# Kernel optimization log

Measured on AMD Instinct MI355X. Metric: run time of the kernel, lower is better.

Reference implementation:

```python
import jax, jax.numpy as jnp
import numpy as np

# Geometry of the single LocallyConnected2d layer being decomposed
FACTOR = 2      # number of sublayers the out_channels are split into
KH = KW = 3     # kernel size
DH = DW = 1     # stride
OH = OW = 32    # output spatial size
B, C_IN, C_OUT = 128, 32, 64
H = W = OH + KH - 1  # 34 (valid unfold with stride 1)


def setup_inputs() -> dict:
    key = jax.random.key(0)
    kx, kw_, kb = jax.random.split(key, 3)
    x = jax.random.normal(kx, (B, C_IN, H, W), dtype=jnp.float32)
    # per-location weights: (out_ch, in_ch, oh, ow, kh*kw) -- no weight sharing
    weight = jax.random.normal(kw_, (C_OUT, C_IN, OH, OW, KH * KW), dtype=jnp.float32) * 0.05
    bias = jax.random.normal(kb, (C_OUT, OH, OW), dtype=jnp.float32)
    return {"x": x, "weight": weight, "bias": bias}


def _unfold(x):
    # x: (B, C, H, W) -> patches: (B, C, OH, OW, KH*KW)
    # equivalent to torch x.unfold(2,kh,dh).unfold(3,kw,dw).reshape(..., kh*kw)
    cols = [x[:, :, i:i + DH * OH:DH, j:j + DW * OW:DW]
            for i in range(KH) for j in range(KW)]
    return jnp.stack(cols, axis=-1)


def reference(x, weight, bias):
    patches = _unfold(x)  # (B, C, OH, OW, K2)
    new_ch = weight.shape[0] // FACTOR
    outs = []
    for g in range(FACTOR):  # decomposed sublayers, concatenated on channel dim
        w_g = weight[g * new_ch:(g + 1) * new_ch]
        b_g = bias[g * new_ch:(g + 1) * new_ch]
        # out[b,o,i,j] = sum_{c,k} patches[b,c,i,j,k] * w[o,c,i,j,k] + b[o,i,j]
        o_g = jnp.einsum('bcijk,ocijk->boij', patches, w_g) + b_g[None]
        outs.append(o_g)
    return jnp.concatenate(outs, axis=1)  # (B, C_OUT, OH, OW)
```

## Files before the change

kernel.cpp:

```cpp
#include <hip/hip_runtime.h>
#include <cstdint>
#include <cstddef>

#define B_    128
#define C_    32
#define O_    64
#define H_    34
#define NPOS  1024
#define K9    9
#define BC    (B_ * C_)
#define BO    (B_ * O_)

typedef __bf16 v8bf __attribute__((ext_vector_type(8)));
typedef float  v4f  __attribute__((ext_vector_type(4)));
typedef float  f4a  __attribute__((ext_vector_type(4)));

__device__ __forceinline__ unsigned short f2bf(float f) {
    union { float f; unsigned int u; } v; v.f = f;
    unsigned int u = v.u;
    return (unsigned short)((u + 0x7FFFu + ((u >> 16) & 1u)) >> 16);
}

__global__ __launch_bounds__(256) void repack_x(const float* __restrict__ x,
                                                unsigned short* __restrict__ x2) {
    const int bq = blockIdx.x / 17;
    const int hp = blockIdx.x % 17;
    const int b0 = bq * 2;
    const int h0 = hp * 2;
    __shared__ unsigned short tile[2][H_][66];
    const int t = threadIdx.x;

    for (int e = t; e < 2176; e += 256) {
        const int bb  = e / 1088;
        const int rem = e % 1088;
        const int c   = rem / 34;
        const int wp  = rem % 34;
        const float2 v = *(const float2*)(x +
            ((size_t)((b0 + bb) * C_ + c) * H_ + h0) * H_ + wp * 2);
        const int hh = (wp >= 17) ? 1 : 0;
        const int w  = wp * 2 - hh * 34;
        const int idx = bb * 32 + c;
        tile[hh][w][idx]     = f2bf(v.x);
        tile[hh][w + 1][idx] = f2bf(v.y);
    }
    __syncthreads();

    for (int e = t; e < 2176; e += 256) {
        const int hh  = e / 1088;
        const int rem = e % 1088;
        const int w   = rem >> 5;
        const int i2  = rem & 31;
        ushort2 pk;
        pk.x = tile[hh][w][i2 * 2];
        pk.y = tile[hh][w][i2 * 2 + 1];
        *(ushort2*)(x2 + (size_t)((h0 + hh) * H_ + w) * BC + bq * 64 + i2 * 2) = pk;
    }
}

__global__ __launch_bounds__(256, 2) void lc_fused2(const unsigned short* __restrict__ x2,
                                                    const float* __restrict__ weight,
                                                    const float* __restrict__ bias,
                                                    float* __restrict__ out) {
    __shared__ __align__(16) unsigned short Wl[72 * 512];

    const int bid = blockIdx.x;
    const int lb  = (bid & 7) * 64 + (bid >> 3);
    const int i   = lb >> 4;
    const int jq  = (lb >> 2) & 3;
    const int oq  = lb & 3;
    const int j0  = jq * 8;
    const int o0  = oq * 16;
    const int posbase = i * 32 + j0;
    const int t = threadIdx.x;

    const float* wbase = weight + ((size_t)(o0 * C_) * NPOS + posbase) * K9;
#pragma unroll
    for (int r = 0; r < 9; ++r) {
        const int idx = r * 256 + t;
        const int plq = idx / 18;
        const int d4  = idx % 18;
        f4a v0 = *(const f4a*)(wbase + (size_t)(plq * 4 + 0) * (NPOS * K9) + d4 * 4);
        f4a v1 = *(const f4a*)(wbase + (size_t)(plq * 4 + 1) * (NPOS * K9) + d4 * 4);
        f4a v2 = *(const f4a*)(wbase + (size_t)(plq * 4 + 2) * (NPOS * K9) + d4 * 4);
        f4a v3 = *(const f4a*)(wbase + (size_t)(plq * 4 + 3) * (NPOS * K9) + d4 * 4);
        const int colbase = (((plq >> 1) ^ (d4 & 7)) * 8) + (plq & 1) * 4;
#pragma unroll
        for (int u = 0; u < 4; ++u) {
            ushort4 pk;
            pk.x = f2bf(v0[u]);
            pk.y = f2bf(v1[u]);
            pk.z = f2bf(v2[u]);
            pk.w = f2bf(v3[u]);
            *(ushort4*)&Wl[(d4 * 4 + u) * 512 + colbase] = pk;
        }
    }
    __syncthreads();

    const int wv = t >> 6;
    const int l  = t & 63;
    const int lm = l & 15;
    const int q  = l >> 4;

    v4f acc[8][2];
#pragma unroll
    for (int a = 0; a < 8; ++a)
#pragma unroll
        for (int m = 0; m < 2; ++m) acc[a][m] = (v4f){0.f, 0.f, 0.f, 0.f};

#pragma unroll
    for (int kh = 0; kh < 3; ++kh) {
        v8bf ax[10][2];
        const int rowbase = (i + kh) * H_ + j0;
#pragma unroll
        for (int w6 = 0; w6 < 10; ++w6) {
            const unsigned short* xrow = x2 + (size_t)(rowbase + w6) * BC;
            ax[w6][0] = *(const v8bf*)(xrow + (wv * 32 + lm) * C_ + q * 8);
            ax[w6][1] = *(const v8bf*)(xrow + (wv * 32 + 16 + lm) * C_ + q * 8);
        }
#pragma unroll
        for (int kw = 0; kw < 3; ++kw) {
            const int tap = kh * 3 + kw;
#pragma unroll
            for (int jj = 0; jj < 8; ++jj) {
                const int jk = jj * K9 + tap;
                const int g  = ((lm * 4 + q) ^ ((jk >> 2) & 7)) * 8;
                const v8bf bfr = *(const v8bf*)&Wl[jk * 512 + g];
                acc[jj][0] = __builtin_amdgcn_mfma_f32_16x16x32_bf16(
                    ax[kw + jj][0], bfr, acc[jj][0], 0, 0, 0);
                acc[jj][1] = __builtin_amdgcn_mfma_f32_16x16x32_bf16(
                    ax[kw + jj][1], bfr, acc[jj][1], 0, 0, 0);
            }
        }
    }

    const float* bp = bias + (size_t)(o0 + lm) * NPOS + posbase;
    const f4a bv0 = *(const f4a*)bp;
    const f4a bv1 = *(const f4a*)(bp + 4);
#pragma unroll
    for (int mt = 0; mt < 2; ++mt) {
#pragma unroll
        for (int r2 = 0; r2 < 4; ++r2) {
            const int b = wv * 32 + mt * 16 + q * 4 + r2;
            float* op = out + ((size_t)b * O_ + (o0 + lm)) * NPOS + posbase;
            f4a lo = {acc[0][mt][r2] + bv0[0], acc[1][mt][r2] + bv0[1],
                      acc[2][mt][r2] + bv0[2], acc[3][mt][r2] + bv0[3]};
            f4a hi = {acc[4][mt][r2] + bv1[0], acc[5][mt][r2] + bv1[1],
                      acc[6][mt][r2] + bv1[2], acc[7][mt][r2] + bv1[3]};
            *(f4a*)op       = lo;
            *(f4a*)(op + 4) = hi;
        }
    }
}

__global__ __launch_bounds__(256) void lc_fallback(const float* __restrict__ x,
                                                   const float* __restrict__ weight,
                                                   const float* __restrict__ bias,
                                                   float* __restrict__ out) {
    const int pos = blockIdx.x;
    const int i = pos >> 5, j = pos & 31;
    const int t  = threadIdx.x;
    const int wv = t >> 6;
    const int l  = t & 63;
    const int lm = l & 15;
    const int q  = l >> 4;

    float bv[4];
#pragma unroll
    for (int nt = 0; nt < 4; ++nt)
        bv[nt] = bias[(size_t)(nt * 16 + lm) * NPOS + pos];

    v4f acc[2][4];
#pragma unroll
    for (int a = 0; a < 2; ++a)
#pragma unroll
        for (int n = 0; n < 4; ++n) acc[a][n] = (v4f){0.f, 0.f, 0.f, 0.f};

    for (int k = 0; k < K9; ++k) {
        const int kh = k / 3, kw = k % 3;
        v8bf af[2], bfr[4];
#pragma unroll
        for (int mt = 0; mt < 2; ++mt) {
            const int b = wv * 32 + mt * 16 + lm;
            union { v8bf v; unsigned short s[8]; } u;
#pragma unroll
            for (int cc = 0; cc < 8; ++cc)
                u.s[cc] = f2bf(x[(((size_t)b * C_ + q * 8 + cc) * H_ + (i + kh)) * H_ + (j + kw)]);
            af[mt] = u.v;
        }
#pragma unroll
        for (int nt = 0; nt < 4; ++nt) {
            union { v8bf v; unsigned short s[8]; } u;
#pragma unroll
            for (int cc = 0; cc < 8; ++cc) {
                const int p = (nt * 16 + lm) * C_ + q * 8 + cc;
                u.s[cc] = f2bf(weight[((size_t)p * NPOS + pos) * K9 + k]);
            }
            bfr[nt] = u.v;
        }
#pragma unroll
        for (int mt = 0; mt < 2; ++mt)
#pragma unroll
            for (int nt = 0; nt < 4; ++nt)
                acc[mt][nt] = __builtin_amdgcn_mfma_f32_16x16x32_bf16(
                    af[mt], bfr[nt], acc[mt][nt], 0, 0, 0);
    }
#pragma unroll
    for (int mt = 0; mt < 2; ++mt)
#pragma unroll
        for (int nt = 0; nt < 4; ++nt) {
            const int o = nt * 16 + lm;
#pragma unroll
            for (int r = 0; r < 4; ++r) {
                const int b = wv * 32 + mt * 16 + q * 4 + r;
                out[(size_t)(b * O_ + o) * NPOS + pos] = acc[mt][nt][r] + bv[nt];
            }
        }
}

extern "C" void kernel_launch(void* const* d_in, const int* in_sizes, int n_in,
                              void* d_out, int out_size, void* d_ws, size_t ws_size,
                              hipStream_t stream) {
    const float* x      = (const float*)d_in[0];
    const float* weight = (const float*)d_in[1];
    const float* bias   = (const float*)d_in[2];
    float* out          = (float*)d_out;

    const size_t X2B = (size_t)H_ * H_ * BC * sizeof(unsigned short);

    if (ws_size >= X2B) {
        unsigned short* x2 = (unsigned short*)d_ws;
        repack_x<<<64 * 17, 256, 0, stream>>>(x, x2);
        lc_fused2<<<512, 256, 0, stream>>>(x2, weight, bias, out);
    } else {
        lc_fallback<<<NPOS, 256, 0, stream>>>(x, weight, bias, out);
    }
}
```

Baseline: 156.7 us.

## Split fused LC kernel by batch half and stage weights in two phases

Each block now handles half the batch (64 rows) and loads its weight tile in two halves of four output positions, halving shared memory. This allows four blocks per CU and doubles the grid to 1024 blocks to improve latency hiding of the weight stream. The cost is that each weight tile is fetched by two blocks, relying on cache reuse, plus an extra barrier and scalar LDS stores.

Measured after the change: 174.2 us. 1.11x slower.

```diff
diff --git a/kernel.cpp b/kernel.cpp
--- a/kernel.cpp
+++ b/kernel.cpp
@@ -10,6 +10,7 @@
 #define K9    9
 #define BC    (B_ * C_)
 #define BO    (B_ * O_)
+#define NPK   (NPOS * K9)
 
 typedef __bf16 v8bf __attribute__((ext_vector_type(8)));
 typedef float  v4f  __attribute__((ext_vector_type(4)));
@@ -57,98 +58,98 @@
     }
 }
 
-__global__ __launch_bounds__(256, 2) void lc_fused2(const unsigned short* __restrict__ x2,
+__global__ __launch_bounds__(256, 4) void lc_fused3(const unsigned short* __restrict__ x2,
                                                     const float* __restrict__ weight,
                                                     const float* __restrict__ bias,
                                                     float* __restrict__ out) {
-    __shared__ __align__(16) unsigned short Wl[72 * 512];
+    __shared__ __align__(16) unsigned short Wl[36 * 512];
 
     const int bid = blockIdx.x;
-    const int lb  = (bid & 7) * 64 + (bid >> 3);
-    const int i   = lb >> 4;
-    const int jq  = (lb >> 2) & 3;
-    const int oq  = lb & 3;
+    const int lb  = (bid & 7) * 128 + (bid >> 3);
+    const int i   = lb >> 5;
+    const int jq  = (lb >> 3) & 3;
+    const int oq  = (lb >> 1) & 3;
+    const int bh  = lb & 1;
     const int j0  = jq * 8;
     const int o0  = oq * 16;
     const int posbase = i * 32 + j0;
     const int t = threadIdx.x;
 
-    const float* wbase = weight + ((size_t)(o0 * C_) * NPOS + posbase) * K9;
-#pragma unroll
-    for (int r = 0; r < 9; ++r) {
-        const int idx = r * 256 + t;
-        const int plq = idx / 18;
-        const int d4  = idx % 18;
-        f4a v0 = *(const f4a*)(wbase + (size_t)(plq * 4 + 0) * (NPOS * K9) + d4 * 4);
-        f4a v1 = *(const f4a*)(wbase + (size_t)(plq * 4 + 1) * (NPOS * K9) + d4 * 4);
-        f4a v2 = *(const f4a*)(wbase + (size_t)(plq * 4 + 2) * (NPOS * K9) + d4 * 4);
-        f4a v3 = *(const f4a*)(wbase + (size_t)(plq * 4 + 3) * (NPOS * K9) + d4 * 4);
-        const int colbase = (((plq >> 1) ^ (d4 & 7)) * 8) + (plq & 1) * 4;
-#pragma unroll
-        for (int u = 0; u < 4; ++u) {
-            ushort4 pk;
-            pk.x = f2bf(v0[u]);
-            pk.y = f2bf(v1[u]);
-            pk.z = f2bf(v2[u]);
-            pk.w = f2bf(v3[u]);
-            *(ushort4*)&Wl[(d4 * 4 + u) * 512 + colbase] = pk;
-        }
-    }
-    __syncthreads();
-
     const int wv = t >> 6;
     const int l  = t & 63;
     const int lm = l & 15;
     const int q  = l >> 4;
 
-    v4f acc[8][2];
-#pragma unroll
-    for (int a = 0; a < 8; ++a)
-#pragma unroll
-        for (int m = 0; m < 2; ++m) acc[a][m] = (v4f){0.f, 0.f, 0.f, 0.f};
-
-#pragma unroll
-    for (int kh = 0; kh < 3; ++kh) {
-        v8bf ax[10][2];
-        const int rowbase = (i + kh) * H_ + j0;
-#pragma unroll
-        for (int w6 = 0; w6 < 10; ++w6) {
-            const unsigned short* xrow = x2 + (size_t)(rowbase + w6) * BC;
-            ax[w6][0] = *(const v8bf*)(xrow + (wv * 32 + lm) * C_ + q * 8);
-            ax[w6][1] = *(const v8bf*)(xrow + (wv * 32 + 16 + lm) * C_ + q * 8);
-        }
-#pragma unroll
-        for (int kw = 0; kw < 3; ++kw) {
-            const int tap = kh * 3 + kw;
-#pragma unroll
-            for (int jj = 0; jj < 8; ++jj) {
-                const int jk = jj * K9 + tap;
-                const int g  = ((lm * 4 + q) ^ ((jk >> 2) & 7)) * 8;
-                const v8bf bfr = *(const v8bf*)&Wl[jk * 512 + g];
-                acc[jj][0] = __builtin_amdgcn_mfma_f32_16x16x32_bf16(
-                    ax[kw + jj][0], bfr, acc[jj][0], 0, 0, 0);
-                acc[jj][1] = __builtin_amdgcn_mfma_f32_16x16x32_bf16(
-                    ax[kw + jj][1], bfr, acc[jj][1], 0, 0, 0);
-            }
-        }
+    v4f acc[8];
+#pragma unroll
+    for (int a = 0; a < 8; ++a) acc[a] = (v4f){0.f, 0.f, 0.f, 0.f};
+
+    const float* wbase = weight + ((size_t)(o0 * C_) * NPOS + posbase) * K9;
+
+#pragma unroll
+    for (int jjh = 0; jjh < 2; ++jjh) {
+        const float* wb = wbase + jjh * 36;
+#pragma unroll
+        for (int g = 0; g < 2; ++g) {
+            f4a v[9];
+#pragma unroll
+            for (int r = 0; r < 9; ++r) {
+                const int idx = (g * 9 + r) * 256 + t;
+                const int pl  = idx / 9;
+                const int d4  = idx % 9;
+                v[r] = *(const f4a*)(wb + (size_t)pl * NPK + d4 * 4);
+            }
+#pragma unroll
+            for (int r = 0; r < 9; ++r) {
+                const int idx = (g * 9 + r) * 256 + t;
+                const int pl  = idx / 9;
+                const int d4  = idx % 9;
+                const int col = ((pl >> 3) ^ (d4 & 7)) * 8 + (pl & 7);
+#pragma unroll
+                for (int u = 0; u < 4; ++u)
+                    Wl[(d4 * 4 + u) * 512 + col] = f2bf(v[r][u]);
+            }
+        }
+        __syncthreads();
+
+#pragma unroll
+        for (int kh = 0; kh < 3; ++kh) {
+            v8bf ax[6];
+            const int rowbase = (i + kh) * H_ + j0 + jjh * 4;
+#pragma unroll
+            for (int w6 = 0; w6 < 6; ++w6) {
+                const unsigned short* xrow = x2 + (size_t)(rowbase + w6) * BC;
+                ax[w6] = *(const v8bf*)(xrow + (bh * 64 + wv * 16 + lm) * C_ + q * 8);
+            }
+#pragma unroll
+            for (int kw = 0; kw < 3; ++kw) {
+                const int tap = kh * 3 + kw;
+#pragma unroll
+                for (int jj = 0; jj < 4; ++jj) {
+                    const int jk = jj * K9 + tap;
+                    const int gc = ((lm * 4 + q) ^ ((jk >> 2) & 7)) * 8;
+                    const v8bf bfr = *(const v8bf*)&Wl[jk * 512 + gc];
+                    acc[jjh * 4 + jj] = __builtin_amdgcn_mfma_f32_16x16x32_bf16(
+                        ax[kw + jj], bfr, acc[jjh * 4 + jj], 0, 0, 0);
+                }
+            }
+        }
+        if (jjh == 0) __syncthreads();
     }
 
     const float* bp = bias + (size_t)(o0 + lm) * NPOS + posbase;
     const f4a bv0 = *(const f4a*)bp;
     const f4a bv1 = *(const f4a*)(bp + 4);
 #pragma unroll
-    for (int mt = 0; mt < 2; ++mt) {
-#pragma unroll
-        for (int r2 = 0; r2 < 4; ++r2) {
-            const int b = wv * 32 + mt * 16 + q * 4 + r2;
-            float* op = out + ((size_t)b * O_ + (o0 + lm)) * NPOS + posbase;
-            f4a lo = {acc[0][mt][r2] + bv0[0], acc[1][mt][r2] + bv0[1],
-                      acc[2][mt][r2] + bv0[2], acc[3][mt][r2] + bv0[3]};
-            f4a hi = {acc[4][mt][r2] + bv1[0], acc[5][mt][r2] + bv1[1],
-                      acc[6][mt][r2] + bv1[2], acc[7][mt][r2] + bv1[3]};
-            *(f4a*)op       = lo;
-            *(f4a*)(op + 4) = hi;
-        }
+    for (int r2 = 0; r2 < 4; ++r2) {
+        const int b = bh * 64 + wv * 16 + q * 4 + r2;
+        float* op = out + ((size_t)b * O_ + (o0 + lm)) * NPOS + posbase;
+        f4a lo = {acc[0][r2] + bv0[0], acc[1][r2] + bv0[1],
+                  acc[2][r2] + bv0[2], acc[3][r2] + bv0[3]};
+        f4a hi = {acc[4][r2] + bv1[0], acc[5][r2] + bv1[1],
+                  acc[6][r2] + bv1[2], acc[7][r2] + bv1[3]};
+        *(f4a*)op       = lo;
+        *(f4a*)(op + 4) = hi;
     }
 }
 
@@ -230,7 +231,7 @@
     if (ws_size >= X2B) {
         unsigned short* x2 = (unsigned short*)d_ws;
         repack_x<<<64 * 17, 256, 0, stream>>>(x, x2);
-        lc_fused2<<<512, 256, 0, stream>>>(x2, weight, bias, out);
+        lc_fused3<<<1024, 256, 0, stream>>>(x2, weight, bias, out);
     } else {
         lc_fallback<<<NPOS, 256, 0, stream>>>(x, weight, bias, out);
     }
```

## Halve weight LDS tile by staging two column halves for higher occupancy

Applied to the files above, without the earlier changes.

The fused kernel now stages the per-position weights into shared memory in two halves of four output columns each, cutting LDS from 72KB to 36KB and raising the launch bound to four blocks per CU. Each half is loaded, converted to bf16 and swizzled, then consumed by MFMAs, with an extra barrier between halves. The aim is more resident waves to hide global-load latency. The cost is re-reading overlapping x rows per half, an added sync, and tighter register limits that could cause spills.

Result: slower. 164.2 us (+4.8%).

```diff
diff --git a/kernel.cpp b/kernel.cpp
--- a/kernel.cpp
+++ b/kernel.cpp
@@ -10,6 +10,7 @@
 #define K9    9
 #define BC    (B_ * C_)
 #define BO    (B_ * O_)
+#define NPK   (NPOS * K9)
 
 typedef __bf16 v8bf __attribute__((ext_vector_type(8)));
 typedef float  v4f  __attribute__((ext_vector_type(4)));
@@ -57,11 +58,11 @@
     }
 }
 
-__global__ __launch_bounds__(256, 2) void lc_fused2(const unsigned short* __restrict__ x2,
+__global__ __launch_bounds__(256, 4) void lc_fused4(const unsigned short* __restrict__ x2,
                                                     const float* __restrict__ weight,
                                                     const float* __restrict__ bias,
                                                     float* __restrict__ out) {
-    __shared__ __align__(16) unsigned short Wl[72 * 512];
+    __shared__ __align__(16) unsigned short Wl[36 * 512];
 
     const int bid = blockIdx.x;
     const int lb  = (bid & 7) * 64 + (bid >> 3);
@@ -73,29 +74,6 @@
     const int posbase = i * 32 + j0;
     const int t = threadIdx.x;
 
-    const float* wbase = weight + ((size_t)(o0 * C_) * NPOS + posbase) * K9;
-#pragma unroll
-    for (int r = 0; r < 9; ++r) {
-        const int idx = r * 256 + t;
-        const int plq = idx / 18;
-        const int d4  = idx % 18;
-        f4a v0 = *(const f4a*)(wbase + (size_t)(plq * 4 + 0) * (NPOS * K9) + d4 * 4);
-        f4a v1 = *(const f4a*)(wbase + (size_t)(plq * 4 + 1) * (NPOS * K9) + d4 * 4);
-        f4a v2 = *(const f4a*)(wbase + (size_t)(plq * 4 + 2) * (NPOS * K9) + d4 * 4);
-        f4a v3 = *(const f4a*)(wbase + (size_t)(plq * 4 + 3) * (NPOS * K9) + d4 * 4);
-        const int colbase = (((plq >> 1) ^ (d4 & 7)) * 8) + (plq & 1) * 4;
-#pragma unroll
-        for (int u = 0; u < 4; ++u) {
-            ushort4 pk;
-            pk.x = f2bf(v0[u]);
-            pk.y = f2bf(v1[u]);
-            pk.z = f2bf(v2[u]);
-            pk.w = f2bf(v3[u]);
-            *(ushort4*)&Wl[(d4 * 4 + u) * 512 + colbase] = pk;
-        }
-    }
-    __syncthreads();
-
     const int wv = t >> 6;
     const int l  = t & 63;
     const int lm = l & 15;
@@ -107,30 +85,81 @@
 #pragma unroll
         for (int m = 0; m < 2; ++m) acc[a][m] = (v4f){0.f, 0.f, 0.f, 0.f};
 
-#pragma unroll
-    for (int kh = 0; kh < 3; ++kh) {
-        v8bf ax[10][2];
-        const int rowbase = (i + kh) * H_ + j0;
-#pragma unroll
-        for (int w6 = 0; w6 < 10; ++w6) {
-            const unsigned short* xrow = x2 + (size_t)(rowbase + w6) * BC;
-            ax[w6][0] = *(const v8bf*)(xrow + (wv * 32 + lm) * C_ + q * 8);
-            ax[w6][1] = *(const v8bf*)(xrow + (wv * 32 + 16 + lm) * C_ + q * 8);
-        }
-#pragma unroll
-        for (int kw = 0; kw < 3; ++kw) {
-            const int tap = kh * 3 + kw;
-#pragma unroll
-            for (int jj = 0; jj < 8; ++jj) {
-                const int jk = jj * K9 + tap;
-                const int g  = ((lm * 4 + q) ^ ((jk >> 2) & 7)) * 8;
-                const v8bf bfr = *(const v8bf*)&Wl[jk * 512 + g];
-                acc[jj][0] = __builtin_amdgcn_mfma_f32_16x16x32_bf16(
-                    ax[kw + jj][0], bfr, acc[jj][0], 0, 0, 0);
-                acc[jj][1] = __builtin_amdgcn_mfma_f32_16x16x32_bf16(
-                    ax[kw + jj][1], bfr, acc[jj][1], 0, 0, 0);
-            }
-        }
+    const float* wbase = weight + ((size_t)(o0 * C_) * NPOS + posbase) * K9;
+
+#pragma unroll
+    for (int jjh = 0; jjh < 2; ++jjh) {
+        const float* wb = wbase + jjh * 36;
+        f4a va[4][2];
+#pragma unroll
+        for (int r = 0; r < 4; ++r) {
+            const int idx = r * 256 + t;
+            const int plp = idx / 9;
+            const int d4  = idx % 9;
+            va[r][0] = *(const f4a*)(wb + (size_t)(plp * 2)     * NPK + d4 * 4);
+            va[r][1] = *(const f4a*)(wb + (size_t)(plp * 2 + 1) * NPK + d4 * 4);
+        }
+        f4a vb[5][2];
+#pragma unroll
+        for (int r = 0; r < 5; ++r) {
+            const int idx = (r + 4) * 256 + t;
+            const int plp = idx / 9;
+            const int d4  = idx % 9;
+            vb[r][0] = *(const f4a*)(wb + (size_t)(plp * 2)     * NPK + d4 * 4);
+            vb[r][1] = *(const f4a*)(wb + (size_t)(plp * 2 + 1) * NPK + d4 * 4);
+        }
+#pragma unroll
+        for (int r = 0; r < 4; ++r) {
+            const int idx = r * 256 + t;
+            const int plp = idx / 9;
+            const int d4  = idx % 9;
+            const int col = (((plp >> 2) ^ (d4 & 7)) << 3) + ((plp & 3) << 1);
+#pragma unroll
+            for (int u = 0; u < 4; ++u) {
+                ushort2 pk; pk.x = f2bf(va[r][0][u]); pk.y = f2bf(va[r][1][u]);
+                *(ushort2*)&Wl[(d4 * 4 + u) * 512 + col] = pk;
+            }
+        }
+#pragma unroll
+        for (int r = 0; r < 5; ++r) {
+            const int idx = (r + 4) * 256 + t;
+            const int plp = idx / 9;
+            const int d4  = idx % 9;
+            const int col = (((plp >> 2) ^ (d4 & 7)) << 3) + ((plp & 3) << 1);
+#pragma unroll
+            for (int u = 0; u < 4; ++u) {
+                ushort2 pk; pk.x = f2bf(vb[r][0][u]); pk.y = f2bf(vb[r][1][u]);
+                *(ushort2*)&Wl[(d4 * 4 + u) * 512 + col] = pk;
+            }
+        }
+        __syncthreads();
+
+#pragma unroll
+        for (int kh = 0; kh < 3; ++kh) {
+            v8bf ax[6][2];
+            const int rowbase = (i + kh) * H_ + j0 + jjh * 4;
+#pragma unroll
+            for (int w6 = 0; w6 < 6; ++w6) {
+                const unsigned short* xrow = x2 + (size_t)(rowbase + w6) * BC;
+                ax[w6][0] = *(const v8bf*)(xrow + (wv * 32 + lm) * C_ + q * 8);
+                ax[w6][1] = *(const v8bf*)(xrow + (wv * 32 + 16 + lm) * C_ + q * 8);
+            }
+#pragma unroll
+            for (int kw = 0; kw < 3; ++kw) {
+                const int tap = kh * 3 + kw;
+#pragma unroll
+                for (int jj = 0; jj < 4; ++jj) {
+                    const int jk = jj * K9 + tap;
+                    const int gc = ((lm * 4 + q) ^ ((jk >> 2) & 7)) * 8;
+                    const v8bf bfr = *(const v8bf*)&Wl[jk * 512 + gc];
+                    acc[jjh * 4 + jj][0] = __builtin_amdgcn_mfma_f32_16x16x32_bf16(
+                        ax[kw + jj][0], bfr, acc[jjh * 4 + jj][0], 0, 0, 0);
+                    acc[jjh * 4 + jj][1] = __builtin_amdgcn_mfma_f32_16x16x32_bf16(
+                        ax[kw + jj][1], bfr, acc[jjh * 4 + jj][1], 0, 0, 0);
+                }
+            }
+        }
+        if (jjh == 0) __syncthreads();
     }
 
     const float* bp = bias + (size_t)(o0 + lm) * NPOS + posbase;
@@ -230,7 +259,7 @@
     if (ws_size >= X2B) {
         unsigned short* x2 = (unsigned short*)d_ws;
         repack_x<<<64 * 17, 256, 0, stream>>>(x, x2);
-        lc_fused2<<<512, 256, 0, stream>>>(x2, weight, bias, out);
+        lc_fused4<<<512, 256, 0, stream>>>(x2, weight, bias, out);
     } else {
         lc_fallback<<<NPOS, 256, 0, stream>>>(x, weight, bias, out);
     }
```
